# Kernel optimization log

Hardware: AMD Instinct MI355X
Metric: run time of the kernel (lower is better)

The kernel has to match this reference:

```python
import jax, jax.numpy as jnp
import numpy as np

B, C, N = 8, 3, 4096
NSAMPLE = 10
MLP = (64, 64)
# checkerboard re-gather pattern from the original module
INDS = np.array([0, 1, 2, 3, 2, 3, 4, 5, 4, 5, 6, 7, 6, 7, 8, 9])


def setup_inputs() -> dict:
    key = jax.random.key(0)
    k1, k2, k3 = jax.random.split(key, 3)
    pos = jax.random.normal(k1, (B, C, N), jnp.float32)
    w1 = jax.random.normal(k2, (MLP[0], 4 * C, 2, 2), jnp.float32) * 0.1  # Conv2d(12, mlp0, k=2)
    b1 = jnp.zeros((MLP[0],), jnp.float32)
    w2 = jax.random.normal(k3, (MLP[1], MLP[0]), jnp.float32) * 0.1       # Conv2d(mlp0, mlp1, k=1)
    b2 = jnp.zeros((MLP[1],), jnp.float32)
    return {"pos": pos, "w1": w1, "b1": b1, "w2": w2, "b2": b2}


def _squeeze_2x2_alt(x):
    # x: [B, N, c, 4, 4] -> [B, N, 4c, 2, 2] with channel order [a, d, b, c]
    a = x[..., 0::2, 0::2]  # (0,0) of each 2x2 block
    d = x[..., 1::2, 1::2]  # (1,1)
    b = x[..., 0::2, 1::2]  # (0,1)
    c = x[..., 1::2, 0::2]  # (1,0)
    return jnp.concatenate([a, d, b, c], axis=-3)


def reference(pos, w1, b1, w2, b2):
    Bn, Cn, Nn = pos.shape
    pos_t = pos.transpose(0, 2, 1)  # [B, N, C]
    # pairwise squared distances [B, N, N]
    sq = jnp.sum(pos_t * pos_t, axis=-1)
    d2 = sq[:, :, None] - 2.0 * jnp.einsum('bnc,bmc->bnm', pos_t, pos_t) + sq[:, None, :]
    _, idx = jax.lax.top_k(-d2, NSAMPLE)  # [B, N, K] nearest neighbors (self first)
    # grouping_operation: grouped[b,c,n,k] = pos[b,c,idx[b,n,k]]
    grouped = jax.vmap(lambda p, i: p[:, i])(pos, idx)  # [B, C, N, K]
    pg = grouped[..., INDS]                              # [B, C, N, 16]
    pg = pg.transpose(0, 2, 1, 3).reshape(Bn, Nn, Cn, 4, 4)  # [B, N, 3, 4, 4]
    sqz = _squeeze_2x2_alt(pg)                           # [B, N, 12, 2, 2]
    # Conv2d(12->mlp0, k=2, stride=1) over 2x2 spatial == full contraction
    h = jnp.einsum('bnchw,ochw->bno', sqz, w1) + b1      # [B, N, mlp0]
    out = jnp.einsum('bno,po->bnp', h, w2) + b2          # [B, N, mlp1]
    return out.transpose(0, 2, 1)                        # [B, mlp1, N]
```

## Files before the change

### kernel.cpp

```cpp
#include <hip/hip_runtime.h>
#include <math.h>

#define NPTS 4096
#define NSMP 10

typedef float f32x2 __attribute__((ext_vector_type(2)));

__global__ __launch_bounds__(256) void prep_kernel(
    const float* __restrict__ w1, const float* __restrict__ b1,
    const float* __restrict__ w2, const float* __restrict__ b2,
    float* __restrict__ wn, float* __restrict__ bb) {
  __shared__ float w1l[64 * 48];
  __shared__ float w2t[64 * 64];
  __shared__ float b1l[64];
  __shared__ float part[4][30][64];
  __shared__ float bpart[4][64];
  const int t = threadIdx.x, p = t & 63, grp = t >> 6, o0 = grp * 16;
  for (int idx = t; idx < 64 * 48; idx += 256) w1l[idx] = w1[idx];
  for (int idx = t; idx < 64 * 64; idx += 256) w2t[(idx & 63) * 64 + (idx >> 6)] = w2[idx];
  if (t < 64) b1l[t] = b1[t];
  __syncthreads();

  const int sg[16] = {0,2,4,6, 3,5,7,9, 1,3,5,7, 2,4,6,8};
  float w2r[16];
  #pragma unroll
  for (int oo = 0; oo < 16; ++oo) w2r[oo] = w2t[(o0 + oo) * 64 + p];
  float wloc[30];
  #pragma unroll
  for (int i = 0; i < 30; ++i) wloc[i] = 0.0f;
  #pragma unroll
  for (int g = 0; g < 4; ++g)
    #pragma unroll
    for (int i = 0; i < 2; ++i)
      #pragma unroll
      for (int j = 0; j < 2; ++j) {
        const int s = sg[g * 4 + i * 2 + j];
        #pragma unroll
        for (int c = 0; c < 3; ++c) {
          const int k = (c + 3 * g) * 4 + i * 2 + j;
          float wk = 0.0f;
          #pragma unroll
          for (int oo = 0; oo < 16; ++oo)
            wk = fmaf(w2r[oo], w1l[(o0 + oo) * 48 + k], wk);
          wloc[s * 3 + c] += wk;
        }
      }
  #pragma unroll
  for (int i = 0; i < 30; ++i) part[grp][i][p] = wloc[i];
  float sb = 0.0f;
  #pragma unroll
  for (int oo = 0; oo < 16; ++oo) sb = fmaf(w2r[oo], b1l[o0 + oo], sb);
  bpart[grp][p] = sb;
  __syncthreads();
  const float* p0 = &part[0][0][0];
  for (int idx = t; idx < 30 * 64; idx += 256)
    wn[idx] = p0[idx] + p0[1920 + idx] + p0[3840 + idx] + p0[5760 + idx];
  if (t < 64) bb[t] = b2[t] + bpart[0][t] + bpart[1][t] + bpart[2][t] + bpart[3][t];
}

__global__ __launch_bounds__(1024, 4) void topk_kernel(const float* __restrict__ pos,
                                                       const float* __restrict__ wng,
                                                       const float* __restrict__ bbg,
                                                       float* __restrict__ out) {
  __shared__ float4 pts[NPTS];
  __shared__ int cnt[16][8];
  __shared__ int bufi[16][8][64];
  __shared__ int nbrL[16][8][NSMP];

  const int b = blockIdx.y, tid = threadIdx.x, lane = tid & 63, wv = tid >> 6;
  const float* pb = pos + (size_t)b * 3 * NPTS;
  for (int i = tid; i < NPTS; i += 1024) {
    float x = pb[i], y = pb[i + NPTS], z = pb[i + 2 * NPTS];
    float sq = __fadd_rn(__fadd_rn(__fmul_rn(x, x), __fmul_rn(y, y)), __fmul_rn(z, z));
    pts[i] = make_float4(x, y, z, sq);
  }
  float wnr[30];
  #pragma unroll
  for (int sc = 0; sc < 30; ++sc) wnr[sc] = wng[sc * 64 + lane];
  const float blv = bbg[lane];
  __syncthreads();

  const int n0 = blockIdx.x * 128 + wv * 8;

  f32x2 qx2[4], qy2[4], qz2[4], dmin[4];
  #pragma unroll
  for (int pp = 0; pp < 4; ++pp) {
    float4 qa = pts[n0 + 2 * pp], qb = pts[n0 + 2 * pp + 1];
    qx2[pp].x = -2.0f * qa.x; qx2[pp].y = -2.0f * qb.x;
    qy2[pp].x = -2.0f * qa.y; qy2[pp].y = -2.0f * qb.y;
    qz2[pp].x = -2.0f * qa.z; qz2[pp].y = -2.0f * qb.z;
    dmin[pp].x = INFINITY; dmin[pp].y = INFINITY;
  }

  #pragma unroll 8
  for (int k = 0; k < 64; ++k) {
    float4 p = pts[k * 64 + lane];
    #pragma unroll
    for (int pp = 0; pp < 4; ++pp) {
      f32x2 key = qx2[pp] * p.x + p.w;
      key = qy2[pp] * p.y + key;
      key = qz2[pp] * p.z + key;
      dmin[pp] = __builtin_elementwise_min(dmin[pp], key);
    }
  }

  unsigned um[8], lo[8], hi[8];
  #pragma unroll
  for (int r = 0; r < 8; ++r) {
    float dm = (r & 1) ? dmin[r >> 1].y : dmin[r >> 1].x;
    unsigned ub = __float_as_uint(dm);
    um[r] = (ub & 0x80000000u) ? ~ub : (ub | 0x80000000u);
    lo[r] = 0u; hi[r] = 0xFFFFFFFFu;
  }
  #pragma unroll 1
  for (int it = 0; it < 20; ++it) {
    #pragma unroll
    for (int r = 0; r < 8; ++r) {
      unsigned mid = lo[r] + ((hi[r] - lo[r]) >> 1);
      int c10 = __popcll(__ballot(um[r] <= mid));
      if (c10 >= NSMP) hi[r] = mid; else lo[r] = mid + 1;
    }
  }
  float tx[8];
  #pragma unroll
  for (int r = 0; r < 8; ++r) {
    unsigned tb = (hi[r] & 0x80000000u) ? (hi[r] ^ 0x80000000u) : ~hi[r];
    float tf = __uint_as_float(tb);
    tx[r] = __fadd_rn(__fadd_rn(tf, 2e-4f), __fmul_rn(fabsf(tf), 1e-5f));
  }

  if (lane < 8) cnt[wv][lane] = 0;

  #pragma unroll 4
  for (int k = 0; k < 64; ++k) {
    float4 p = pts[k * 64 + lane];
    #pragma unroll
    for (int pp = 0; pp < 4; ++pp) {
      f32x2 key = qx2[pp] * p.x + p.w;
      key = qy2[pp] * p.y + key;
      key = qz2[pp] * p.z + key;
      if (key.x <= tx[2 * pp]) {
        int ps = atomicAdd(&cnt[wv][2 * pp], 1);
        if (ps < 64) bufi[wv][2 * pp][ps] = k * 64 + lane;
      }
      if (key.y <= tx[2 * pp + 1]) {
        int ps = atomicAdd(&cnt[wv][2 * pp + 1], 1);
        if (ps < 64) bufi[wv][2 * pp + 1][ps] = k * 64 + lane;
      }
    }
  }

  int c[8], si[8], rank[8];
  double dd[8];
  int cmax = 0;
  #pragma unroll
  for (int r = 0; r < 8; ++r) {
    c[r] = __builtin_amdgcn_readfirstlane(cnt[wv][r]);
    if (c[r] > 64) c[r] = 64;
    cmax = (c[r] > cmax) ? c[r] : cmax;
    rank[r] = 0;
  }
  #pragma unroll
  for (int r = 0; r < 8; ++r) {
    float4 qa = pts[n0 + r];
    if (lane < c[r]) {
      si[r] = bufi[wv][r][lane];
      float4 p = pts[si[r]];
      double dqx = (double)qa.x, dqy = (double)qa.y, dqz = (double)qa.z;
      double px = (double)p.x, py = (double)p.y, pz = (double)p.z;
      double dot = dqx * px + dqy * py + dqz * pz;
      double sqn = dqx * dqx + dqy * dqy + dqz * dqz;
      double sqm = px * px + py * py + pz * pz;
      dd[r] = (sqn - 2.0 * dot) + sqm;
    } else { dd[r] = (double)INFINITY; si[r] = 0x7FFFFFFF; }
  }
  #pragma unroll 1
  for (int j = 0; j < cmax; ++j) {
    #pragma unroll
    for (int r = 0; r < 8; ++r) {
      int jlo = __builtin_amdgcn_readlane(__double2loint(dd[r]), j);
      int jhi = __builtin_amdgcn_readlane(__double2hiint(dd[r]), j);
      int ji  = __builtin_amdgcn_readlane(si[r], j);
      double jd = __hiloint2double(jhi, jlo);
      if (jd < dd[r] || (jd == dd[r] && ji < si[r])) ++rank[r];
    }
  }
  #pragma unroll
  for (int r = 0; r < 8; ++r)
    if (lane < c[r] && rank[r] < NSMP)
      nbrL[wv][r][rank[r]] = si[r];

  float acc[8];
  #pragma unroll
  for (int r = 0; r < 8; ++r) acc[r] = blv;
  #pragma unroll 1
  for (int r = 0; r < 8; ++r) {
    float a = acc[r];
    #pragma unroll
    for (int s = 0; s < NSMP; ++s) {
      int id = nbrL[wv][r][s];
      float4 pv = pts[id];
      a = fmaf(wnr[s * 3 + 0], pv.x, a);
      a = fmaf(wnr[s * 3 + 1], pv.y, a);
      a = fmaf(wnr[s * 3 + 2], pv.z, a);
    }
    acc[r] = a;
  }
  float* ob = out + ((size_t)b * 64 + lane) * NPTS + n0;
  float4 v0 = make_float4(acc[0], acc[1], acc[2], acc[3]);
  float4 v1 = make_float4(acc[4], acc[5], acc[6], acc[7]);
  *(float4*)(ob)     = v0;
  *(float4*)(ob + 4) = v1;
}

extern "C" void kernel_launch(void* const* d_in, const int* in_sizes, int n_in,
                              void* d_out, int out_size, void* d_ws, size_t ws_size,
                              hipStream_t stream) {
  (void)in_sizes; (void)n_in; (void)out_size; (void)ws_size;
  const float* pos = (const float*)d_in[0];
  const float* w1  = (const float*)d_in[1];
  const float* b1  = (const float*)d_in[2];
  const float* w2  = (const float*)d_in[3];
  const float* b2  = (const float*)d_in[4];
  float* out = (float*)d_out;

  float* wn = (float*)d_ws;
  float* bb = (float*)((char*)d_ws + 30 * 64 * 4);

  prep_kernel<<<dim3(1), dim3(256), 0, stream>>>(w1, b1, w2, b2, wn, bb);
  topk_kernel<<<dim3(32, 8), dim3(1024), 0, stream>>>(pos, wn, bb, out);
}
```

Baseline: 135.7 us.

## Halve queries per wave, pack points as xyz in LDS, transpose output via LDS

Each wave now handles 4 query points instead of 8, and the grid doubles to 64x8 blocks, giving more blocks across the GPU. Points are stored in LDS as packed xyz without the precomputed squared norm, which is recomputed per candidate. Weights live in LDS instead of registers to cut register pressure, and output goes through an LDS transpose so that stores are coalesced rows of 64 points. This trades extra norm FMAs, strided LDS reads and a block-wide barrier for higher occupancy and better-coalesced writes. The bisection now runs 24 iterations instead of 20.

```diff
diff --git a/kernel.cpp b/kernel.cpp
--- a/kernel.cpp
+++ b/kernel.cpp
@@ -58,126 +58,136 @@
   if (t < 64) bb[t] = b2[t] + bpart[0][t] + bpart[1][t] + bpart[2][t] + bpart[3][t];
 }
 
-__global__ __launch_bounds__(1024, 4) void topk_kernel(const float* __restrict__ pos,
+__global__ __launch_bounds__(1024, 8) void topk_kernel(const float* __restrict__ pos,
                                                        const float* __restrict__ wng,
                                                        const float* __restrict__ bbg,
                                                        float* __restrict__ out) {
-  __shared__ float4 pts[NPTS];
-  __shared__ int cnt[16][8];
-  __shared__ int bufi[16][8][64];
-  __shared__ int nbrL[16][8][NSMP];
+  __shared__ float pts3[NPTS * 3];
+  __shared__ float trans[16 * 260];
+  __shared__ float wl[30 * 64];
+  __shared__ float bl[64];
+  __shared__ int   nbrL[16][4][NSMP];
+  __shared__ int   cnt[16][4];
 
   const int b = blockIdx.y, tid = threadIdx.x, lane = tid & 63, wv = tid >> 6;
   const float* pb = pos + (size_t)b * 3 * NPTS;
   for (int i = tid; i < NPTS; i += 1024) {
-    float x = pb[i], y = pb[i + NPTS], z = pb[i + 2 * NPTS];
-    float sq = __fadd_rn(__fadd_rn(__fmul_rn(x, x), __fmul_rn(y, y)), __fmul_rn(z, z));
-    pts[i] = make_float4(x, y, z, sq);
-  }
-  float wnr[30];
-  #pragma unroll
-  for (int sc = 0; sc < 30; ++sc) wnr[sc] = wng[sc * 64 + lane];
-  const float blv = bbg[lane];
-  __syncthreads();
-
-  const int n0 = blockIdx.x * 128 + wv * 8;
-
-  f32x2 qx2[4], qy2[4], qz2[4], dmin[4];
-  #pragma unroll
-  for (int pp = 0; pp < 4; ++pp) {
-    float4 qa = pts[n0 + 2 * pp], qb = pts[n0 + 2 * pp + 1];
-    qx2[pp].x = -2.0f * qa.x; qx2[pp].y = -2.0f * qb.x;
-    qy2[pp].x = -2.0f * qa.y; qy2[pp].y = -2.0f * qb.y;
-    qz2[pp].x = -2.0f * qa.z; qz2[pp].y = -2.0f * qb.z;
+    pts3[3 * i + 0] = pb[i];
+    pts3[3 * i + 1] = pb[i + NPTS];
+    pts3[3 * i + 2] = pb[i + 2 * NPTS];
+  }
+  for (int i = tid; i < 30 * 64; i += 1024) wl[i] = wng[i];
+  if (tid < 64) bl[tid] = bbg[tid];
+  __syncthreads();
+
+  const int nb = blockIdx.x * 64;
+  const int n0 = nb + wv * 4;
+  float* transF = &trans[wv * 260];
+  int*   bufiW  = (int*)transF;
+
+  f32x2 qx2[2], qy2[2], qz2[2], dmin[2];
+  #pragma unroll
+  for (int pp = 0; pp < 2; ++pp) {
+    int na = n0 + 2 * pp;
+    qx2[pp].x = -2.0f * pts3[3 * na + 0]; qx2[pp].y = -2.0f * pts3[3 * na + 3];
+    qy2[pp].x = -2.0f * pts3[3 * na + 1]; qy2[pp].y = -2.0f * pts3[3 * na + 4];
+    qz2[pp].x = -2.0f * pts3[3 * na + 2]; qz2[pp].y = -2.0f * pts3[3 * na + 5];
     dmin[pp].x = INFINITY; dmin[pp].y = INFINITY;
   }
 
-  #pragma unroll 8
+  #pragma unroll 4
   for (int k = 0; k < 64; ++k) {
-    float4 p = pts[k * 64 + lane];
-    #pragma unroll
-    for (int pp = 0; pp < 4; ++pp) {
-      f32x2 key = qx2[pp] * p.x + p.w;
-      key = qy2[pp] * p.y + key;
-      key = qz2[pp] * p.z + key;
+    int m = k * 64 + lane;
+    float x = pts3[3 * m], y = pts3[3 * m + 1], z = pts3[3 * m + 2];
+    float sq = fmaf(z, z, fmaf(y, y, x * x));
+    f32x2 sq2; sq2.x = sq; sq2.y = sq;
+    #pragma unroll
+    for (int pp = 0; pp < 2; ++pp) {
+      f32x2 key = qx2[pp] * x + sq2;
+      key = qy2[pp] * y + key;
+      key = qz2[pp] * z + key;
       dmin[pp] = __builtin_elementwise_min(dmin[pp], key);
     }
   }
 
-  unsigned um[8], lo[8], hi[8];
-  #pragma unroll
-  for (int r = 0; r < 8; ++r) {
+  unsigned um[4], lo[4], hi[4];
+  #pragma unroll
+  for (int r = 0; r < 4; ++r) {
     float dm = (r & 1) ? dmin[r >> 1].y : dmin[r >> 1].x;
     unsigned ub = __float_as_uint(dm);
     um[r] = (ub & 0x80000000u) ? ~ub : (ub | 0x80000000u);
     lo[r] = 0u; hi[r] = 0xFFFFFFFFu;
   }
   #pragma unroll 1
-  for (int it = 0; it < 20; ++it) {
-    #pragma unroll
-    for (int r = 0; r < 8; ++r) {
+  for (int it = 0; it < 24; ++it) {
+    #pragma unroll
+    for (int r = 0; r < 4; ++r) {
       unsigned mid = lo[r] + ((hi[r] - lo[r]) >> 1);
       int c10 = __popcll(__ballot(um[r] <= mid));
       if (c10 >= NSMP) hi[r] = mid; else lo[r] = mid + 1;
     }
   }
-  float tx[8];
-  #pragma unroll
-  for (int r = 0; r < 8; ++r) {
+  float tx[4];
+  #pragma unroll
+  for (int r = 0; r < 4; ++r) {
     unsigned tb = (hi[r] & 0x80000000u) ? (hi[r] ^ 0x80000000u) : ~hi[r];
     float tf = __uint_as_float(tb);
     tx[r] = __fadd_rn(__fadd_rn(tf, 2e-4f), __fmul_rn(fabsf(tf), 1e-5f));
   }
 
-  if (lane < 8) cnt[wv][lane] = 0;
+  if (lane < 4) cnt[wv][lane] = 0;
 
   #pragma unroll 4
   for (int k = 0; k < 64; ++k) {
-    float4 p = pts[k * 64 + lane];
-    #pragma unroll
-    for (int pp = 0; pp < 4; ++pp) {
-      f32x2 key = qx2[pp] * p.x + p.w;
-      key = qy2[pp] * p.y + key;
-      key = qz2[pp] * p.z + key;
+    int m = k * 64 + lane;
+    float x = pts3[3 * m], y = pts3[3 * m + 1], z = pts3[3 * m + 2];
+    float sq = fmaf(z, z, fmaf(y, y, x * x));
+    f32x2 sq2; sq2.x = sq; sq2.y = sq;
+    #pragma unroll
+    for (int pp = 0; pp < 2; ++pp) {
+      f32x2 key = qx2[pp] * x + sq2;
+      key = qy2[pp] * y + key;
+      key = qz2[pp] * z + key;
       if (key.x <= tx[2 * pp]) {
         int ps = atomicAdd(&cnt[wv][2 * pp], 1);
-        if (ps < 64) bufi[wv][2 * pp][ps] = k * 64 + lane;
+        if (ps < 64) bufiW[(2 * pp) * 64 + ps] = m;
       }
       if (key.y <= tx[2 * pp + 1]) {
         int ps = atomicAdd(&cnt[wv][2 * pp + 1], 1);
-        if (ps < 64) bufi[wv][2 * pp + 1][ps] = k * 64 + lane;
+        if (ps < 64) bufiW[(2 * pp + 1) * 64 + ps] = m;
       }
     }
   }
 
-  int c[8], si[8], rank[8];
-  double dd[8];
+  int c[4], si[4], rank[4];
+  double dd[4];
   int cmax = 0;
   #pragma unroll
-  for (int r = 0; r < 8; ++r) {
+  for (int r = 0; r < 4; ++r) {
     c[r] = __builtin_amdgcn_readfirstlane(cnt[wv][r]);
     if (c[r] > 64) c[r] = 64;
     cmax = (c[r] > cmax) ? c[r] : cmax;
     rank[r] = 0;
   }
   #pragma unroll
-  for (int r = 0; r < 8; ++r) {
-    float4 qa = pts[n0 + r];
+  for (int r = 0; r < 4; ++r) {
+    int nq = n0 + r;
+    float qxf = pts3[3 * nq], qyf = pts3[3 * nq + 1], qzf = pts3[3 * nq + 2];
     if (lane < c[r]) {
-      si[r] = bufi[wv][r][lane];
-      float4 p = pts[si[r]];
-      double dqx = (double)qa.x, dqy = (double)qa.y, dqz = (double)qa.z;
-      double px = (double)p.x, py = (double)p.y, pz = (double)p.z;
-      double dot = dqx * px + dqy * py + dqz * pz;
+      si[r] = bufiW[r * 64 + lane];
+      float px = pts3[3 * si[r]], py = pts3[3 * si[r] + 1], pz = pts3[3 * si[r] + 2];
+      double dqx = (double)qxf, dqy = (double)qyf, dqz = (double)qzf;
+      double dpx = (double)px, dpy = (double)py, dpz = (double)pz;
+      double dot = dqx * dpx + dqy * dpy + dqz * dpz;
       double sqn = dqx * dqx + dqy * dqy + dqz * dqz;
-      double sqm = px * px + py * py + pz * pz;
+      double sqm = dpx * dpx + dpy * dpy + dpz * dpz;
       dd[r] = (sqn - 2.0 * dot) + sqm;
     } else { dd[r] = (double)INFINITY; si[r] = 0x7FFFFFFF; }
   }
   #pragma unroll 1
   for (int j = 0; j < cmax; ++j) {
     #pragma unroll
-    for (int r = 0; r < 8; ++r) {
+    for (int r = 0; r < 4; ++r) {
       int jlo = __builtin_amdgcn_readlane(__double2loint(dd[r]), j);
       int jhi = __builtin_amdgcn_readlane(__double2hiint(dd[r]), j);
       int ji  = __builtin_amdgcn_readlane(si[r], j);
@@ -186,31 +196,34 @@
     }
   }
   #pragma unroll
-  for (int r = 0; r < 8; ++r)
+  for (int r = 0; r < 4; ++r)
     if (lane < c[r] && rank[r] < NSMP)
       nbrL[wv][r][rank[r]] = si[r];
 
-  float acc[8];
-  #pragma unroll
-  for (int r = 0; r < 8; ++r) acc[r] = blv;
   #pragma unroll 1
-  for (int r = 0; r < 8; ++r) {
-    float a = acc[r];
+  for (int r = 0; r < 4; ++r) {
+    float a = bl[lane];
     #pragma unroll
     for (int s = 0; s < NSMP; ++s) {
       int id = nbrL[wv][r][s];
-      float4 pv = pts[id];
-      a = fmaf(wnr[s * 3 + 0], pv.x, a);
-      a = fmaf(wnr[s * 3 + 1], pv.y, a);
-      a = fmaf(wnr[s * 3 + 2], pv.z, a);
-    }
-    acc[r] = a;
-  }
-  float* ob = out + ((size_t)b * 64 + lane) * NPTS + n0;
-  float4 v0 = make_float4(acc[0], acc[1], acc[2], acc[3]);
-  float4 v1 = make_float4(acc[4], acc[5], acc[6], acc[7]);
-  *(float4*)(ob)     = v0;
-  *(float4*)(ob + 4) = v1;
+      float px = pts3[3 * id], py = pts3[3 * id + 1], pz = pts3[3 * id + 2];
+      a = fmaf(wl[(s * 3 + 0) * 64 + lane], px, a);
+      a = fmaf(wl[(s * 3 + 1) * 64 + lane], py, a);
+      a = fmaf(wl[(s * 3 + 2) * 64 + lane], pz, a);
+    }
+    transF[r * 65 + lane] = a;
+  }
+  __syncthreads();
+
+  {
+    int p = tid >> 4, t16 = tid & 15;
+    float4 v;
+    v.x = trans[t16 * 260 + 0 * 65 + p];
+    v.y = trans[t16 * 260 + 1 * 65 + p];
+    v.z = trans[t16 * 260 + 2 * 65 + p];
+    v.w = trans[t16 * 260 + 3 * 65 + p];
+    *(float4*)(out + ((size_t)b * 64 + p) * NPTS + nb + 4 * t16) = v;
+  }
 }
 
 extern "C" void kernel_launch(void* const* d_in, const int* in_sizes, int n_in,
@@ -228,5 +241,5 @@
   float* bb = (float*)((char*)d_ws + 30 * 64 * 4);
 
   prep_kernel<<<dim3(1), dim3(256), 0, stream>>>(w1, b1, w2, b2, wn, bb);
-  topk_kernel<<<dim3(32, 8), dim3(1024), 0, stream>>>(pos, wn, bb, out);
+  topk_kernel<<<dim3(64, 8), dim3(1024), 0, stream>>>(pos, wn, bb, out);
 }
```

Result: no change. 133.8 us (-1.4%).
